# Kernel optimization log

Measured on AMD Instinct MI355X. Metric: run time of the kernel, lower is better.

## Reference

```python
import jax, jax.numpy as jnp
import numpy as np


def setup_inputs() -> dict:
    key = jax.random.key(0)
    ks = jax.random.split(key, 7)
    B, C, W, H = 4, 128, 64, 64
    Cq = C // 8
    x = jax.random.normal(ks[0], (B, C, W, H), jnp.float32)
    wq = jax.random.normal(ks[1], (Cq, C), jnp.float32) * 0.05
    bq = jax.random.normal(ks[2], (Cq,), jnp.float32) * 0.05
    wk = jax.random.normal(ks[3], (Cq, C), jnp.float32) * 0.05
    bk = jax.random.normal(ks[4], (Cq,), jnp.float32) * 0.05
    wv = jax.random.normal(ks[5], (C, C), jnp.float32) * 0.05
    bv = jax.random.normal(ks[6], (C,), jnp.float32) * 0.05
    gamma = jnp.ones((1,), jnp.float32)
    return {"x": x, "wq": wq, "bq": bq, "wk": wk, "bk": bk,
            "wv": wv, "bv": bv, "gamma": gamma}


def reference(x, wq, bq, wk, bk, wv, bv, gamma):
    B, C, W, H = x.shape
    N = W * H
    xf = x.reshape(B, C, N)  # flatten spatial dims (W fastest over H, as torch .view)
    # 1x1 convs == per-position linear maps
    q = jnp.einsum('dc,bcn->bnd', wq, xf) + bq            # [B, N, C//8]
    k = jnp.einsum('dc,bcn->bdn', wk, xf) + bk[:, None]   # [B, C//8, N]
    v = jnp.einsum('dc,bcn->bdn', wv, xf) + bv[:, None]   # [B, C, N]
    energy = jnp.einsum('bnd,bdm->bnm', q, k)             # [B, N, N]
    # block-causal mask: position i may attend only to j < (i//W + 1)*W
    i = jnp.arange(N)
    j = jnp.arange(N)
    masked = j[None, :] >= ((i[:, None] // W) + 1) * W    # True -> -inf
    energy = jnp.where(masked[None, :, :], -jnp.inf, energy)
    attention = jax.nn.softmax(energy, axis=-1)           # [B, N, N]
    # out[b,c,n] = sum_m V[b,c,m] * attn[b,n,m]  (torch bmm(V, attn^T))
    out = jnp.einsum('bcm,bnm->bcn', v, attention).reshape(B, C, W, H)
    out = gamma * out + x
    return (out, attention)
```

## Files before the change

### kernel.cpp

```cpp
#include <hip/hip_runtime.h>
#include <hip/hip_bf16.h>


typedef __attribute__((ext_vector_type(8))) short short8;
typedef __attribute__((ext_vector_type(16))) float float16;

__device__ __forceinline__ ushort f2bf(float f) {
  union { float f; uint u; } v; v.f = f;
  return (ushort)((v.u + 0x7FFFu + ((v.u >> 16) & 1u)) >> 16);
}

__global__ __launch_bounds__(512, 2) void qkv_kernel(
    const float* __restrict__ x,
    const float* __restrict__ wq, const float* __restrict__ bq,
    const float* __restrict__ wk, const float* __restrict__ bk,
    const float* __restrict__ wv, const float* __restrict__ bv,
    ushort* __restrict__ qT, ushort* __restrict__ kT, ushort* __restrict__ vo) {
  __shared__ float xs[128 * 64];
  const int nt = blockIdx.x, b = blockIdx.y;
  const int n0 = nt * 64;
  const float* xb = x + (size_t)b * 524288 + n0;
  for (int idx = threadIdx.x; idx < 8192; idx += 512) {
    int c = idx >> 6, n = idx & 63;
    xs[idx] = xb[(size_t)c * 4096 + n];
  }
  __syncthreads();
  const int n = threadIdx.x & 63;
  const int og = __builtin_amdgcn_readfirstlane((int)(threadIdx.x >> 6));
  float acc[20];
#pragma unroll
  for (int i = 0; i < 20; i++) {
    int o = og + 8 * i;
    acc[i] = (i < 2) ? bq[o] : (i < 4) ? bk[o - 16] : bv[o - 32];
  }
#pragma unroll 4
  for (int c = 0; c < 128; c++) {
    float xr = xs[c * 64 + n];
#pragma unroll
    for (int i = 0; i < 20; i++) {
      int o = og + 8 * i;
      const float* wr = (i < 2) ? (wq + o * 128)
                      : (i < 4) ? (wk + (o - 16) * 128)
                                : (wv + (o - 32) * 128);
      acc[i] += wr[c] * xr;
    }
  }
  const size_t pos = (size_t)b * 4096 + n0 + n;
#pragma unroll
  for (int i = 0; i < 20; i++) {
    int o = og + 8 * i;
    if (i < 2)      qT[pos * 16 + o]      = f2bf(acc[i]);
    else if (i < 4) kT[pos * 16 + o - 16] = f2bf(acc[i]);
    else vo[(size_t)b * 524288 + (size_t)(o - 32) * 4096 + n0 + n] = f2bf(acc[i]);
  }
}

__global__ __launch_bounds__(256, 2) void fused_attn_kernel(
    const ushort* __restrict__ qT, const ushort* __restrict__ kT,
    const ushort* __restrict__ vws, const float* __restrict__ x,
    const float* __restrict__ g,
    float* __restrict__ attn, float* __restrict__ out) {
  __shared__ __align__(16) ushort Pt[4][32 * 72];
  __shared__ __align__(16) float red[32][4];
  const int bx = blockIdx.x;
  const int b = bx & 3;
  const int v_ = bx >> 2;
  const int half = v_ & 1;
  const int u = v_ >> 1;
  const int rb = (u < 32) ? u : 95 - u;
  const int S = rb + 1;
  const int lane = threadIdx.x & 63;
  const int w = __builtin_amdgcn_readfirstlane((int)(threadIdx.x >> 6));
  const int nblk = rb * 64 + half * 32;
  const int l31 = lane & 31;
  const int h = lane >> 5;
  const int hk = h * 8;
  const ushort* qb = qT + (size_t)b * 65536;
  const ushort* kb = kT + (size_t)b * 65536;
  const ushort* vp = vws + (size_t)b * 524288;
  float* ab = attn + (size_t)b * 16777216;

  const short8 qa = *(const short8*)(qb + (size_t)(nblk + l31) * 16 + hk);

  float16 zero16;
#pragma unroll
  for (int i = 0; i < 16; i++) zero16[i] = 0.f;

  float sume[16];
#pragma unroll
  for (int i = 0; i < 16; i++) sume[i] = 0.f;
  for (int s = w; s < S; s += 4) {
    const int m0 = s * 64;
#pragma unroll
    for (int mh = 0; mh < 2; mh++) {
      short8 kf = *(const short8*)(kb + (size_t)(m0 + mh * 32 + l31) * 16 + hk);
      float16 e = __builtin_amdgcn_mfma_f32_32x32x16_bf16(qa, kf, zero16, 0, 0, 0);
#pragma unroll
      for (int r = 0; r < 16; r++) sume[r] += __expf(e[r]);
    }
  }
#pragma unroll
  for (int r = 0; r < 16; r++) {
#pragma unroll
    for (int off = 1; off <= 16; off <<= 1)
      sume[r] += __shfl_xor(sume[r], off, 64);
  }
  if (l31 == 0) {
#pragma unroll
    for (int r = 0; r < 16; r++) {
      int row = (r & 3) + 8 * (r >> 2) + 4 * h;
      red[row][w] = sume[r];
    }
  }
  __syncthreads();
  float inv[16];
#pragma unroll
  for (int r = 0; r < 16; r++) {
    int row = (r & 3) + 8 * (r >> 2) + 4 * h;
    float4 p4 = *(const float4*)&red[row][0];
    inv[r] = 1.0f / (p4.x + p4.y + p4.z + p4.w);
  }

  float16 acc = zero16;
  for (int s0 = 0; s0 < S; s0 += 4) {
    const int sl = (S - s0 < 4) ? (S - s0) : 4;
    if (w < sl) {
      const int m0 = (s0 + w) * 64;
      ushort* Pb = &Pt[w][0];
#pragma unroll
      for (int mh = 0; mh < 2; mh++) {
        short8 kf = *(const short8*)(kb + (size_t)(m0 + mh * 32 + l31) * 16 + hk);
        float16 e = __builtin_amdgcn_mfma_f32_32x32x16_bf16(qa, kf, zero16, 0, 0, 0);
#pragma unroll
        for (int r = 0; r < 16; r++) {
          int row = (r & 3) + 8 * (r >> 2) + 4 * h;
          float p = __expf(e[r]) * inv[r];
          ab[(size_t)(nblk + row) * 4096 + m0 + mh * 32 + l31] = p;
          Pb[row * 72 + mh * 32 + l31] = f2bf(p);
        }
      }
    }
    __syncthreads();
    for (int ss = 0; ss < sl; ss++) {
      const int m0 = (s0 + ss) * 64;
      const ushort* vrow = vp + (size_t)(w * 32 + l31) * 4096 + m0 + hk;
      const ushort* Pr = &Pt[ss][l31 * 72 + hk];
#pragma unroll
      for (int kk = 0; kk < 4; kk++) {
        short8 a  = *(const short8*)(vrow + kk * 16);
        short8 bf = *(const short8*)(Pr + kk * 16);
        acc = __builtin_amdgcn_mfma_f32_32x32x16_bf16(a, bf, acc, 0, 0, 0);
      }
    }
    __syncthreads();
  }

  const int M = S * 64;
  const int Z4 = (4096 - M) >> 2;
  const float4 z = make_float4(0.f, 0.f, 0.f, 0.f);
#pragma unroll
  for (int r = 0; r < 8; r++) {
    float4* dst = (float4*)(ab + (size_t)(nblk + w * 8 + r) * 4096 + M);
    for (int i4 = lane; i4 < Z4; i4 += 64) dst[i4] = z;
  }

  const float gamma = g[0];
#pragma unroll
  for (int reg = 0; reg < 16; reg++) {
    int row = (reg & 3) + 8 * (reg >> 2) + 4 * h;
    int c = w * 32 + row;
    int n = nblk + l31;
    size_t off = (size_t)b * 524288 + (size_t)c * 4096 + n;
    out[off] = gamma * acc[reg] + x[off];
  }
}

extern "C" void kernel_launch(void* const* d_in, const int* in_sizes, int n_in,
                              void* d_out, int out_size, void* d_ws, size_t ws_size,
                              hipStream_t stream) {
  const float* x  = (const float*)d_in[0];
  const float* wq = (const float*)d_in[1];
  const float* bq = (const float*)d_in[2];
  const float* wk = (const float*)d_in[3];
  const float* bk = (const float*)d_in[4];
  const float* wv = (const float*)d_in[5];
  const float* bv = (const float*)d_in[6];
  const float* gm = (const float*)d_in[7];
  float* out  = (float*)d_out;
  float* attn = out + 2097152;
  ushort* qTw = (ushort*)d_ws;
  ushort* kTw = qTw + 262144;
  ushort* vws = qTw + 524288;

  qkv_kernel<<<dim3(64, 4), 512, 0, stream>>>(x, wq, bq, wk, bk, wv, bv, qTw, kTw, vws);
  fused_attn_kernel<<<dim3(512), 256, 0, stream>>>(qTw, kTw, vws, x, gm, attn, out);
}
```

Baseline: 350.3 us.

## Split fused attention into denominator, attention-write, and PV kernels

Splits the single fused attention kernel into three launches. One computes the softmax denominators into a workspace. One writes the full attention matrix, including the zero fill, using twice as many blocks and nontemporal stores. The last recomputes P and does the PV MFMA plus the residual. The aim is to separate the large store-bound attention write from the compute-bound PV path so each gets its own parallelism and occupancy. The cost is two extra launches and recomputing QK^T/exp in three places.

```diff
diff --git a/kernel.cpp b/kernel.cpp
--- a/kernel.cpp
+++ b/kernel.cpp
@@ -4,6 +4,7 @@
 
 typedef __attribute__((ext_vector_type(8))) short short8;
 typedef __attribute__((ext_vector_type(16))) float float16;
+typedef __attribute__((ext_vector_type(4))) float floatx4;
 
 __device__ __forceinline__ ushort f2bf(float f) {
   union { float f; uint u; } v; v.f = f;
@@ -55,13 +56,137 @@
   }
 }
 
-__global__ __launch_bounds__(256, 2) void fused_attn_kernel(
+__global__ __launch_bounds__(256, 2) void denom_kernel(
     const ushort* __restrict__ qT, const ushort* __restrict__ kT,
-    const ushort* __restrict__ vws, const float* __restrict__ x,
-    const float* __restrict__ g,
-    float* __restrict__ attn, float* __restrict__ out) {
+    float* __restrict__ invw) {
+  __shared__ float red[32][4];
+  const int bx = blockIdx.x;
+  const int b = bx & 3;
+  const int v_ = bx >> 2;
+  const int half = v_ & 1;
+  const int u = v_ >> 1;
+  const int rb = (u < 32) ? u : 95 - u;
+  const int S = rb + 1;
+  const int lane = threadIdx.x & 63;
+  const int w = __builtin_amdgcn_readfirstlane((int)(threadIdx.x >> 6));
+  const int nblk = rb * 64 + half * 32;
+  const int l31 = lane & 31;
+  const int h = lane >> 5;
+  const int hk = h * 8;
+  const ushort* qb = qT + (size_t)b * 65536;
+  const ushort* kb = kT + (size_t)b * 65536;
+  const short8 qa = *(const short8*)(qb + (size_t)(nblk + l31) * 16 + hk);
+  float16 zero16;
+#pragma unroll
+  for (int i = 0; i < 16; i++) zero16[i] = 0.f;
+
+  float sume[16];
+#pragma unroll
+  for (int i = 0; i < 16; i++) sume[i] = 0.f;
+  for (int s = w; s < S; s += 4) {
+    const int m0 = s * 64;
+#pragma unroll
+    for (int mh = 0; mh < 2; mh++) {
+      short8 kf = *(const short8*)(kb + (size_t)(m0 + mh * 32 + l31) * 16 + hk);
+      float16 e = __builtin_amdgcn_mfma_f32_32x32x16_bf16(qa, kf, zero16, 0, 0, 0);
+#pragma unroll
+      for (int r = 0; r < 16; r++) sume[r] += __expf(e[r]);
+    }
+  }
+#pragma unroll
+  for (int r = 0; r < 16; r++) {
+#pragma unroll
+    for (int off = 1; off <= 16; off <<= 1)
+      sume[r] += __shfl_xor(sume[r], off, 64);
+  }
+  if (l31 == 0) {
+#pragma unroll
+    for (int r = 0; r < 16; r++) {
+      int row = (r & 3) + 8 * (r >> 2) + 4 * h;
+      red[row][w] = sume[r];
+    }
+  }
+  __syncthreads();
+  if (w == 0 && l31 == 0) {
+#pragma unroll
+    for (int r = 0; r < 16; r++) {
+      int row = (r & 3) + 8 * (r >> 2) + 4 * h;
+      float4 p4 = *(const float4*)&red[row][0];
+      invw[(size_t)b * 4096 + nblk + row] = 1.0f / (p4.x + p4.y + p4.z + p4.w);
+    }
+  }
+}
+
+__global__ __launch_bounds__(256, 4) void attn_write_kernel(
+    const ushort* __restrict__ qT, const ushort* __restrict__ kT,
+    const float* __restrict__ invw, float* __restrict__ attn) {
+  const int bx = blockIdx.x;
+  const int b = bx & 3;
+  const int ch = (bx >> 2) & 1;
+  const int v_ = bx >> 3;
+  const int half = v_ & 1;
+  const int u = v_ >> 1;
+  const int rb = (u < 32) ? u : 95 - u;
+  const int S = rb + 1;
+  const int M = S * 64;
+  const int lane = threadIdx.x & 63;
+  const int w = __builtin_amdgcn_readfirstlane((int)(threadIdx.x >> 6));
+  const int nblk = rb * 64 + half * 32;
+  const int l31 = lane & 31;
+  const int h = lane >> 5;
+  const int hk = h * 8;
+  const ushort* qb = qT + (size_t)b * 65536;
+  const ushort* kb = kT + (size_t)b * 65536;
+  float* ab = attn + (size_t)b * 16777216;
+
+  const short8 qa = *(const short8*)(qb + (size_t)(nblk + l31) * 16 + hk);
+  float inv_r[16];
+#pragma unroll
+  for (int r = 0; r < 16; r++) {
+    int row = (r & 3) + 8 * (r >> 2) + 4 * h;
+    inv_r[r] = invw[(size_t)b * 4096 + nblk + row];
+  }
+  float16 zero16;
+#pragma unroll
+  for (int i = 0; i < 16; i++) zero16[i] = 0.f;
+
+  const int sEnd = (S < ch * 32 + 32) ? S : (ch * 32 + 32);
+  for (int s = ch * 32 + w; s < sEnd; s += 4) {
+    const int m0 = s * 64;
+#pragma unroll
+    for (int mh = 0; mh < 2; mh++) {
+      short8 kf = *(const short8*)(kb + (size_t)(m0 + mh * 32 + l31) * 16 + hk);
+      float16 e = __builtin_amdgcn_mfma_f32_32x32x16_bf16(qa, kf, zero16, 0, 0, 0);
+#pragma unroll
+      for (int r = 0; r < 16; r++) {
+        int row = (r & 3) + 8 * (r >> 2) + 4 * h;
+        float p = __expf(e[r]) * inv_r[r];
+        __builtin_nontemporal_store(
+            p, &ab[(size_t)(nblk + row) * 4096 + m0 + mh * 32 + l31]);
+      }
+    }
+  }
+
+  const int zc0 = (M > ch * 2048) ? M : ch * 2048;
+  const int zc1 = (ch + 1) * 2048;
+  if (zc0 < zc1) {
+    const int Z4 = (zc1 - zc0) >> 2;
+    const floatx4 z = {0.f, 0.f, 0.f, 0.f};
+#pragma unroll
+    for (int r = 0; r < 8; r++) {
+      floatx4* dst = (floatx4*)(ab + (size_t)(nblk + w * 8 + r) * 4096 + zc0);
+      for (int i4 = lane; i4 < Z4; i4 += 64)
+        __builtin_nontemporal_store(z, &dst[i4]);
+    }
+  }
+}
+
+__global__ __launch_bounds__(256, 2) void pv_kernel(
+    const ushort* __restrict__ qT, const ushort* __restrict__ kT,
+    const ushort* __restrict__ vws, const float* __restrict__ invw,
+    const float* __restrict__ x, const float* __restrict__ g,
+    float* __restrict__ out) {
   __shared__ __align__(16) ushort Pt[4][32 * 72];
-  __shared__ __align__(16) float red[32][4];
   const int bx = blockIdx.x;
   const int b = bx & 3;
   const int v_ = bx >> 2;
@@ -78,48 +203,17 @@
   const ushort* qb = qT + (size_t)b * 65536;
   const ushort* kb = kT + (size_t)b * 65536;
   const ushort* vp = vws + (size_t)b * 524288;
-  float* ab = attn + (size_t)b * 16777216;
 
   const short8 qa = *(const short8*)(qb + (size_t)(nblk + l31) * 16 + hk);
-
-  float16 zero16;
-#pragma unroll
-  for (int i = 0; i < 16; i++) zero16[i] = 0.f;
-
-  float sume[16];
-#pragma unroll
-  for (int i = 0; i < 16; i++) sume[i] = 0.f;
-  for (int s = w; s < S; s += 4) {
-    const int m0 = s * 64;
-#pragma unroll
-    for (int mh = 0; mh < 2; mh++) {
-      short8 kf = *(const short8*)(kb + (size_t)(m0 + mh * 32 + l31) * 16 + hk);
-      float16 e = __builtin_amdgcn_mfma_f32_32x32x16_bf16(qa, kf, zero16, 0, 0, 0);
-#pragma unroll
-      for (int r = 0; r < 16; r++) sume[r] += __expf(e[r]);
-    }
-  }
-#pragma unroll
-  for (int r = 0; r < 16; r++) {
-#pragma unroll
-    for (int off = 1; off <= 16; off <<= 1)
-      sume[r] += __shfl_xor(sume[r], off, 64);
-  }
-  if (l31 == 0) {
-#pragma unroll
-    for (int r = 0; r < 16; r++) {
-      int row = (r & 3) + 8 * (r >> 2) + 4 * h;
-      red[row][w] = sume[r];
-    }
-  }
-  __syncthreads();
-  float inv[16];
+  float inv_r[16];
 #pragma unroll
   for (int r = 0; r < 16; r++) {
     int row = (r & 3) + 8 * (r >> 2) + 4 * h;
-    float4 p4 = *(const float4*)&red[row][0];
-    inv[r] = 1.0f / (p4.x + p4.y + p4.z + p4.w);
-  }
+    inv_r[r] = invw[(size_t)b * 4096 + nblk + row];
+  }
+  float16 zero16;
+#pragma unroll
+  for (int i = 0; i < 16; i++) zero16[i] = 0.f;
 
   float16 acc = zero16;
   for (int s0 = 0; s0 < S; s0 += 4) {
@@ -134,8 +228,7 @@
 #pragma unroll
         for (int r = 0; r < 16; r++) {
           int row = (r & 3) + 8 * (r >> 2) + 4 * h;
-          float p = __expf(e[r]) * inv[r];
-          ab[(size_t)(nblk + row) * 4096 + m0 + mh * 32 + l31] = p;
+          float p = __expf(e[r]) * inv_r[r];
           Pb[row * 72 + mh * 32 + l31] = f2bf(p);
         }
       }
@@ -153,15 +246,6 @@
       }
     }
     __syncthreads();
-  }
-
-  const int M = S * 64;
-  const int Z4 = (4096 - M) >> 2;
-  const float4 z = make_float4(0.f, 0.f, 0.f, 0.f);
-#pragma unroll
-  for (int r = 0; r < 8; r++) {
-    float4* dst = (float4*)(ab + (size_t)(nblk + w * 8 + r) * 4096 + M);
-    for (int i4 = lane; i4 < Z4; i4 += 64) dst[i4] = z;
   }
 
   const float gamma = g[0];
@@ -191,7 +275,10 @@
   ushort* qTw = (ushort*)d_ws;
   ushort* kTw = qTw + 262144;
   ushort* vws = qTw + 524288;
+  float* invw = (float*)(qTw + 2621440);
 
   qkv_kernel<<<dim3(64, 4), 512, 0, stream>>>(x, wq, bq, wk, bk, wv, bv, qTw, kTw, vws);
-  fused_attn_kernel<<<dim3(512), 256, 0, stream>>>(qTw, kTw, vws, x, gm, attn, out);
-}
+  denom_kernel<<<dim3(512), 256, 0, stream>>>(qTw, kTw, invw);
+  attn_write_kernel<<<dim3(1024), 256, 0, stream>>>(qTw, kTw, invw, attn);
+  pv_kernel<<<dim3(512), 256, 0, stream>>>(qTw, kTw, vws, invw, x, gm, out);
+}
```

Result: slower. 400.5 us (+14.3%).
